# Kernel tuning notes

Hardware: AMD Instinct MI355X
Metric: run time of the kernel (lower is better)

The kernel has to match this reference:

```python
import jax, jax.numpy as jnp
import numpy as np

X_CH, Y_CH = 3, 31
C = X_CH + Y_CH            # s_channels = m_channels = 34
A = C * (C - 1) // 2       # 561 Givens rotation angles
SMIN, SMAX = 0.001, 1000.0


def setup_inputs() -> dict:
    key = jax.random.key(0)
    k1, k2 = jax.random.split(key)
    x = jax.random.normal(k1, (4, X_CH, 64, 64), dtype=jnp.float32)
    W = jax.random.normal(k2, (C + C + A, X_CH), dtype=jnp.float32) * 0.1
    b = jnp.zeros((C + C + A,), dtype=jnp.float32)
    return {"x": x, "W": W, "b": b}


def _covariance(s, a):
    # s: (B, C, H, W) positive variances; a: (B, A, H, W) rotation angles.
    B, _, H, Wd = s.shape
    cs = jnp.moveaxis(jnp.cos(a), 1, 0)  # (A, B, H, W)
    ss = jnp.moveaxis(jnp.sin(a), 1, 0)  # (A, B, H, W)
    ii, jj = np.triu_indices(C, k=1)      # same (i, j) order as the torch double loop
    ii = jnp.asarray(ii, dtype=jnp.int32)
    jj = jnp.asarray(jj, dtype=jnp.int32)

    # R starts as identity; each Givens rotation rij only mixes columns i and j
    # of R (R <- R @ rij), so we update two columns instead of a full matmul.
    R0 = jnp.broadcast_to(jnp.eye(C, dtype=s.dtype), (B, H, Wd, C, C))

    def step(R, inp):
        c_, s_, i, j = inp
        col_i = R[..., i]                      # (B, H, W, C)
        col_j = R[..., j]
        c_ = c_[..., None]
        s_ = s_[..., None]
        R = R.at[..., i].set(c_ * col_i + s_ * col_j)
        R = R.at[..., j].set(-s_ * col_i + c_ * col_j)
        return R, None

    R, _ = jax.lax.scan(step, R0, (cs, ss, ii, jj))
    sp = jnp.transpose(s, (0, 2, 3, 1))        # (B, H, W, C)
    # S = R^T D R with D = diag(sp): S[k,n] = sum_m R[m,k] * sp[m] * R[m,n]
    S = jnp.einsum('bhwmk,bhwm,bhwmn->bhwkn', R, sp, R)
    D = jnp.zeros((B, H, Wd, C, C), dtype=s.dtype).at[..., jnp.arange(C), jnp.arange(C)].set(sp)
    return S, R, D


def reference(x, W, b):
    # 1x1-conv encoder: (B, 3, H, W) -> (B, 629, H, W)
    w = jnp.einsum('oc,bchw->bohw', W, x) + b[None, :, None, None]
    m = jnp.transpose(w[:, :C], (0, 2, 3, 1))                  # (B, H, W, C) mean
    s = jax.nn.sigmoid(w[:, C:2 * C])
    s = SMIN * (1.0 - s) + SMAX * s                            # (B, C, H, W)
    a = jnp.pi * jnp.tanh(w[:, 2 * C:])                        # (B, A, H, W)
    S, _, _ = _covariance(s, a)
    return m, S, s
```

## Files before the change

### kernel.cpp

```cpp
#include <hip/hip_runtime.h>


#define CCH 34
#define ACH 561
#define HWPIX 4096
#define NPIX 16384
#define PXB 14
#define NTHR 256
#define CH0 281
#define CSPAIR (281 * 16)
#define VROW 36
#define VPX (17 * VROW * 4)
#define OFF_S 557056
#define OFF_s 19496960
#define LOG2E 1.4426950408889634f

typedef float   f32x2 __attribute__((ext_vector_type(2)));
typedef _Float16 h2   __attribute__((ext_vector_type(2)));

struct Pairs {
    short i[ACH]; short j[ACH];
    constexpr Pairs() : i(), j() {
        int p = 0;
        for (int a = 0; a < CCH - 1; ++a)
            for (int b = a + 1; b < CCH; ++b) { i[p] = (short)a; j[p] = (short)b; ++p; }
    }
};
__device__ constexpr Pairs PR{};

__device__ __forceinline__ float dot2h(h2 a, h2 b, float c) {
#if __has_builtin(__builtin_amdgcn_fdot2)
    return __builtin_amdgcn_fdot2(a, b, c, false);
#else
    return fmaf((float)a[0], (float)b[0], fmaf((float)a[1], (float)b[1], c));
#endif
}

__device__ __forceinline__ void rot2(f32x2& Ri, f32x2& Rj, f32x2 c2, f32x2 s2) {
    f32x2 t1, t2;
    asm("v_pk_mul_f32 %0, %1, %2" : "=v"(t1) : "v"(s2), "v"(Rj));
    asm("v_pk_mul_f32 %0, %1, %2" : "=v"(t2) : "v"(s2), "v"(Ri));
    asm("v_pk_fma_f32 %0, %1, %2, %3" : "=v"(Ri) : "v"(c2), "v"(Ri), "v"(t1));
    asm("v_pk_fma_f32 %0, %1, %2, %3 neg_lo:[0,0,1] neg_hi:[0,0,1]"
        : "=v"(Rj) : "v"(c2), "v"(Rj), "v"(t2));
}

template <int P0, int P1>
__device__ __forceinline__ void apply_rots(f32x2* R2, const float4* cs) {
    #pragma unroll
    for (int k = P0; k < P1; ++k) {
        float4 cc = cs[k - P0];
        f32x2 c2; c2[0] = cc.x; c2[1] = cc.y;
        f32x2 s2; s2[0] = cc.z; s2[1] = cc.w;
        rot2(R2[PR.i[k]], R2[PR.j[k]], c2, s2);
    }
}

__device__ __forceinline__ float2 cs_of(float wv) {
    float e  = __builtin_amdgcn_exp2f((2.0f * LOG2E) * wv);
    float tt = 1.0f - 2.0f * __builtin_amdgcn_rcpf(e + 1.0f);
    float rv = 0.5f * tt;
    return make_float2(__builtin_amdgcn_cosf(rv), __builtin_amdgcn_sinf(rv));
}

template <int G0, int LEN>
__device__ __forceinline__ void fill_cs(const float* __restrict__ Wm,
                                        const float* __restrict__ bvec,
                                        const float* xs, char* ldsbuf,
                                        int npr, int npx, int t) {
    for (int o = t; o < npr * LEN; o += NTHR) {
        int pr = (int)((unsigned)o / (unsigned)LEN);
        int l  = o - pr * LEN;
        int ch = 2 * CCH + G0 + l;
        float w0 = Wm[ch * 3 + 0], w1 = Wm[ch * 3 + 1], w2 = Wm[ch * 3 + 2];
        float bb = bvec[ch];
        int pa = 2 * pr;
        int pb = (2 * pr + 1 < npx) ? (2 * pr + 1) : pa;
        float2 A = cs_of(fmaf(w0, xs[pa*3+0], fmaf(w1, xs[pa*3+1], w2 * xs[pa*3+2])) + bb);
        float2 B = cs_of(fmaf(w0, xs[pb*3+0], fmaf(w1, xs[pb*3+1], w2 * xs[pb*3+2])) + bb);
        float4 cell; cell.x = A.x; cell.y = B.x; cell.z = A.y; cell.w = B.y;
        *(float4*)(ldsbuf + pr * CSPAIR + l * 16) = cell;
    }
}

__global__ __launch_bounds__(NTHR, 4) void gpd_kernel(
    const float* __restrict__ x,
    const float* __restrict__ Wm,
    const float* __restrict__ bvec,
    float* __restrict__ out)
{
    __shared__ alignas(16) char ldsbuf[PXB * VPX];
    __shared__ _Float16 lds_sh[PXB * CCH];
    __shared__ float xs[PXB * 3];

    const int t   = threadIdx.x;
    const int p0  = blockIdx.x * PXB;
    const int npx = min(PXB, NPIX - p0);
    const int npr = (npx + 1) >> 1;

    for (int i = t; i < npx * 3; i += NTHR) {
        int px = (int)((unsigned)i / 3u); int c = i - px * 3;
        int p = p0 + px; int b = p >> 12; int hw = p & 4095;
        xs[i] = x[(b * 3 + c) * HWPIX + hw];
    }
    __syncthreads();

    for (int o = t; o < npx * 68; o += NTHR) {
        int q = (int)((unsigned)o / 68u); int ch = o - q * 68;
        int p = p0 + q; int b = p >> 12; int hw = p & 4095;
        float wv = fmaf(Wm[ch*3+0], xs[q*3+0],
                   fmaf(Wm[ch*3+1], xs[q*3+1], Wm[ch*3+2] * xs[q*3+2])) + bvec[ch];
        if (ch < CCH) {
            out[(size_t)p * CCH + ch] = wv;
        } else {
            float e  = __builtin_amdgcn_exp2f(-wv * LOG2E);
            float sg = __builtin_amdgcn_rcpf(1.0f + e);
            float sv = fmaf(999.999f, sg, 0.001f);
            int c = ch - CCH;
            out[OFF_s + (size_t)(b * CCH + c) * HWPIX + hw] = sv;
            lds_sh[q * CCH + c] = (_Float16)sv;
        }
    }

    const int pr = t / CCH;
    const int m  = t - pr * CCH;
    const bool act = (t < npr * CCH);
    const bool hasB = act && (2 * pr + 1 < npx);

    f32x2 R2[CCH];
    #pragma unroll
    for (int k = 0; k < CCH; ++k) { R2[k][0] = (k == m) ? 1.0f : 0.0f; R2[k][1] = R2[k][0]; }

    fill_cs<0, CH0>(Wm, bvec, xs, ldsbuf, npr, npx, t);
    __syncthreads();
    if (act) apply_rots<0, CH0>(R2, (const float4*)(ldsbuf + pr * CSPAIR));
    __syncthreads();
    fill_cs<CH0, ACH - CH0>(Wm, bvec, xs, ldsbuf, npr, npx, t);
    __syncthreads();
    if (act) apply_rots<CH0, ACH>(R2, (const float4*)(ldsbuf + pr * CSPAIR));
    __syncthreads();

    if (act) {
        char* baseA = ldsbuf + (2*pr)   * VPX + (m >> 1) * (VROW*4) + (m & 1) * 2;
        char* baseB = ldsbuf + (2*pr+1) * VPX + (m >> 1) * (VROW*4) + (m & 1) * 2;
        #pragma unroll
        for (int n = 0; n < CCH; ++n) {
#if __has_builtin(__builtin_amdgcn_cvt_pkrtz)
            h2 hv = __builtin_bit_cast(h2, __builtin_amdgcn_cvt_pkrtz(R2[n][0], R2[n][1]));
#else
            h2 hv; hv[0] = (_Float16)R2[n][0]; hv[1] = (_Float16)R2[n][1];
#endif
            *(_Float16*)(baseA + n * 4) = hv[0];
            if (hasB) *(_Float16*)(baseB + n * 4) = hv[1];
        }
    }
    __syncthreads();

    for (int hh = 0; hh < 2; ++hh) {
        int px = 2 * pr + hh;
        if (act && px < npx) {
            const unsigned* base = (const unsigned*)(ldsbuf + px * VPX);
            const _Float16* sh = lds_sh + px * CCH;
            float acc[CCH];
            #pragma unroll
            for (int n = 0; n < CCH; ++n) acc[n] = 0.0f;
            for (int mp = 0; mp < 17; ++mp) {
                const unsigned* row = base + mp * VROW;
                h2 vk = __builtin_bit_cast(h2, row[m]) * *(const h2*)(sh + 2 * mp);
                #pragma unroll
                for (int g = 0; g < 8; ++g) {
                    uint4 rr = *(const uint4*)(row + 4 * g);
                    acc[4*g+0] = dot2h(vk, __builtin_bit_cast(h2, rr.x), acc[4*g+0]);
                    acc[4*g+1] = dot2h(vk, __builtin_bit_cast(h2, rr.y), acc[4*g+1]);
                    acc[4*g+2] = dot2h(vk, __builtin_bit_cast(h2, rr.z), acc[4*g+2]);
                    acc[4*g+3] = dot2h(vk, __builtin_bit_cast(h2, rr.w), acc[4*g+3]);
                }
                uint2 rr2 = *(const uint2*)(row + 32);
                acc[32] = dot2h(vk, __builtin_bit_cast(h2, rr2.x), acc[32]);
                acc[33] = dot2h(vk, __builtin_bit_cast(h2, rr2.y), acc[33]);
            }
            float* os = out + OFF_S + (size_t)(p0 + px) * (CCH * CCH) + m * CCH;
            #pragma unroll
            for (int n2 = 0; n2 < 17; ++n2) {
                float2 v; v.x = acc[2*n2]; v.y = acc[2*n2+1];
                *(float2*)(os + 2 * n2) = v;
            }
        }
    }
}

extern "C" void kernel_launch(void* const* d_in, const int* in_sizes, int n_in,
                              void* d_out, int out_size, void* d_ws, size_t ws_size,
                              hipStream_t stream) {
    const float* x  = (const float*)d_in[0];
    const float* W  = (const float*)d_in[1];
    const float* bv = (const float*)d_in[2];
    float* out = (float*)d_out;
    const int nblk = (NPIX + PXB - 1) / PXB;
    hipLaunchKernelGGL(gpd_kernel, dim3(nblk), dim3(NTHR), 0, stream,
                       x, W, bv, out);
}
```

Before: 78.60 us.

## Halve LDS footprint by chunking rotations into four stages and per-half V staging

The cos/sin staging buffer is cut from two chunks of 281 angles to four chunks of about 140. The R-matrix staging buffer now holds only one pixel per pair at a time, with the two halves processed sequentially. Together these roughly halve shared memory per block so launch bounds can target 5 blocks per CU instead of 4. In exchange it adds more barriers and removes the odd-pixel guard, relying on PXB being even and NPIX dividing evenly.

```diff
diff --git a/kernel.cpp b/kernel.cpp
--- a/kernel.cpp
+++ b/kernel.cpp
@@ -6,17 +6,18 @@
 #define HWPIX 4096
 #define NPIX 16384
 #define PXB 14
+#define NPR 7
 #define NTHR 256
-#define CH0 281
-#define CSPAIR (281 * 16)
+#define CSLEN 141
+#define CSPAIR (CSLEN * 16)
 #define VROW 36
 #define VPX (17 * VROW * 4)
 #define OFF_S 557056
 #define OFF_s 19496960
 #define LOG2E 1.4426950408889634f
 
-typedef float   f32x2 __attribute__((ext_vector_type(2)));
-typedef _Float16 h2   __attribute__((ext_vector_type(2)));
+typedef float    f32x2 __attribute__((ext_vector_type(2)));
+typedef _Float16 h2    __attribute__((ext_vector_type(2)));
 
 struct Pairs {
     short i[ACH]; short j[ACH];
@@ -67,15 +68,14 @@
 __device__ __forceinline__ void fill_cs(const float* __restrict__ Wm,
                                         const float* __restrict__ bvec,
                                         const float* xs, char* ldsbuf,
-                                        int npr, int npx, int t) {
+                                        int npr, int t) {
     for (int o = t; o < npr * LEN; o += NTHR) {
         int pr = (int)((unsigned)o / (unsigned)LEN);
         int l  = o - pr * LEN;
         int ch = 2 * CCH + G0 + l;
         float w0 = Wm[ch * 3 + 0], w1 = Wm[ch * 3 + 1], w2 = Wm[ch * 3 + 2];
         float bb = bvec[ch];
-        int pa = 2 * pr;
-        int pb = (2 * pr + 1 < npx) ? (2 * pr + 1) : pa;
+        int pa = 2 * pr, pb = 2 * pr + 1;
         float2 A = cs_of(fmaf(w0, xs[pa*3+0], fmaf(w1, xs[pa*3+1], w2 * xs[pa*3+2])) + bb);
         float2 B = cs_of(fmaf(w0, xs[pb*3+0], fmaf(w1, xs[pb*3+1], w2 * xs[pb*3+2])) + bb);
         float4 cell; cell.x = A.x; cell.y = B.x; cell.z = A.y; cell.w = B.y;
@@ -83,13 +83,13 @@
     }
 }
 
-__global__ __launch_bounds__(NTHR, 4) void gpd_kernel(
+__global__ __launch_bounds__(NTHR, 5) void gpd_kernel(
     const float* __restrict__ x,
     const float* __restrict__ Wm,
     const float* __restrict__ bvec,
     float* __restrict__ out)
 {
-    __shared__ alignas(16) char ldsbuf[PXB * VPX];
+    __shared__ alignas(16) char ldsbuf[NPR * VPX];
     __shared__ _Float16 lds_sh[PXB * CCH];
     __shared__ float xs[PXB * 3];
 
@@ -125,47 +125,57 @@
     const int pr = t / CCH;
     const int m  = t - pr * CCH;
     const bool act = (t < npr * CCH);
-    const bool hasB = act && (2 * pr + 1 < npx);
 
     f32x2 R2[CCH];
     #pragma unroll
     for (int k = 0; k < CCH; ++k) { R2[k][0] = (k == m) ? 1.0f : 0.0f; R2[k][1] = R2[k][0]; }
 
-    fill_cs<0, CH0>(Wm, bvec, xs, ldsbuf, npr, npx, t);
-    __syncthreads();
-    if (act) apply_rots<0, CH0>(R2, (const float4*)(ldsbuf + pr * CSPAIR));
-    __syncthreads();
-    fill_cs<CH0, ACH - CH0>(Wm, bvec, xs, ldsbuf, npr, npx, t);
-    __syncthreads();
-    if (act) apply_rots<CH0, ACH>(R2, (const float4*)(ldsbuf + pr * CSPAIR));
-    __syncthreads();
-
-    if (act) {
-        char* baseA = ldsbuf + (2*pr)   * VPX + (m >> 1) * (VROW*4) + (m & 1) * 2;
-        char* baseB = ldsbuf + (2*pr+1) * VPX + (m >> 1) * (VROW*4) + (m & 1) * 2;
-        #pragma unroll
-        for (int n = 0; n < CCH; ++n) {
+    fill_cs<0, 141>(Wm, bvec, xs, ldsbuf, npr, t);
+    __syncthreads();
+    if (act) apply_rots<0, 141>(R2, (const float4*)(ldsbuf + pr * CSPAIR));
+    __syncthreads();
+    fill_cs<141, 140>(Wm, bvec, xs, ldsbuf, npr, t);
+    __syncthreads();
+    if (act) apply_rots<141, 281>(R2, (const float4*)(ldsbuf + pr * CSPAIR));
+    __syncthreads();
+    fill_cs<281, 140>(Wm, bvec, xs, ldsbuf, npr, t);
+    __syncthreads();
+    if (act) apply_rots<281, 421>(R2, (const float4*)(ldsbuf + pr * CSPAIR));
+    __syncthreads();
+    fill_cs<421, 140>(Wm, bvec, xs, ldsbuf, npr, t);
+    __syncthreads();
+    if (act) apply_rots<421, 561>(R2, (const float4*)(ldsbuf + pr * CSPAIR));
+    __syncthreads();
+
+    h2 Rh[CCH];
+    #pragma unroll
+    for (int n = 0; n < CCH; ++n) {
 #if __has_builtin(__builtin_amdgcn_cvt_pkrtz)
-            h2 hv = __builtin_bit_cast(h2, __builtin_amdgcn_cvt_pkrtz(R2[n][0], R2[n][1]));
+        Rh[n] = __builtin_bit_cast(h2, __builtin_amdgcn_cvt_pkrtz(R2[n][0], R2[n][1]));
 #else
-            h2 hv; hv[0] = (_Float16)R2[n][0]; hv[1] = (_Float16)R2[n][1];
+        h2 hv; hv[0] = (_Float16)R2[n][0]; hv[1] = (_Float16)R2[n][1]; Rh[n] = hv;
 #endif
-            *(_Float16*)(baseA + n * 4) = hv[0];
-            if (hasB) *(_Float16*)(baseB + n * 4) = hv[1];
+    }
+
+    #pragma unroll
+    for (int h = 0; h < 2; ++h) {
+        if (act) {
+            char* base = ldsbuf + pr * VPX + (m >> 1) * (VROW * 4) + (m & 1) * 2;
+            #pragma unroll
+            for (int n = 0; n < CCH; ++n)
+                *(_Float16*)(base + n * 4) = Rh[n][h];
         }
-    }
-    __syncthreads();
-
-    for (int hh = 0; hh < 2; ++hh) {
-        int px = 2 * pr + hh;
-        if (act && px < npx) {
-            const unsigned* base = (const unsigned*)(ldsbuf + px * VPX);
+        __syncthreads();
+
+        if (act) {
+            const int px = 2 * pr + h;
+            const unsigned* vb = (const unsigned*)(ldsbuf + pr * VPX);
             const _Float16* sh = lds_sh + px * CCH;
             float acc[CCH];
             #pragma unroll
             for (int n = 0; n < CCH; ++n) acc[n] = 0.0f;
             for (int mp = 0; mp < 17; ++mp) {
-                const unsigned* row = base + mp * VROW;
+                const unsigned* row = vb + mp * VROW;
                 h2 vk = __builtin_bit_cast(h2, row[m]) * *(const h2*)(sh + 2 * mp);
                 #pragma unroll
                 for (int g = 0; g < 8; ++g) {
@@ -186,6 +196,7 @@
                 *(float2*)(os + 2 * n2) = v;
             }
         }
+        __syncthreads();
     }
 }
 
```

New measurement: 74.79 us. 4.8% less time.
